# Performance work log

Hardware: AMD Instinct MI355X
Metric: run time of the kernel (lower is better)

The kernel has to match this reference:

```python
import jax, jax.numpy as jnp
import numpy as np

M, N = 63, 127            # parity checks x code length (BCH(127,64))
B = 256                   # base batch of codewords
NUM_SHIFTS = 4            # GL 'num_shifts'
NUM_ITERS = 3             # GL 'num_iterations'
PENALTY = 2.0             # GL 'penalty_weight'
BIG = 1e30

_POS = (2 * np.arange(N)) % N          # Frobenius automorphism i -> 2i mod n
_INV = np.zeros(N, np.int32); _INV[_POS] = np.arange(N)
_STEP = N // NUM_SHIFTS
_SHIFTS = [i * _STEP for i in range(NUM_SHIFTS)]  # deterministic (offset=0)


def setup_inputs() -> dict:
    key = jax.random.key(0)
    k1, k2 = jax.random.split(key)
    soft_input = jax.random.normal(k1, (B, N), dtype=jnp.float32)
    labels = jax.random.randint(k2, (B, N), 0, 2).astype(jnp.int32)
    rng = np.random.default_rng(0)
    Hnp = (rng.random((M, N)) < 0.25).astype(np.float32)
    rows = np.arange(M)
    Hnp[rows, rows % N] = 1.0              # guarantee >=2 ones per check row
    Hnp[rows, (rows + 1) % N] = 1.0
    H = jnp.asarray(Hnp, jnp.float32)
    check_weight = jnp.array([0.421], jnp.float32)
    return {"soft_input": soft_input, "labels": labels, "H": H,
            "check_weight": check_weight}


def _interleave(a, b):
    m, n1 = a.shape
    n2 = b.shape[1]
    if n1 == n2:
        return jnp.stack([a, b], axis=2).reshape(m, n1 + n2)
    inter = jnp.stack([a[:, :n2], b], axis=2).reshape(m, 2 * n2)
    return jnp.concatenate([inter, a[:, n2:]], axis=1)


def _compute_cv(vc, H, check_weight):
    # vc: [Bs, M, N] masked variable->check messages
    sign = jnp.sign((1.0 - H)[None] + vc)
    row_sign = jnp.prod(sign, axis=2, keepdims=True)      # product over row
    result_sign = row_sign * H * sign                     # extrinsic sign
    back = jnp.where(H == 0, -BIG - 1.0, 0.0)[None]
    vabs = jnp.clip(jnp.abs(vc), 0.0, BIG)
    top2 = jax.lax.top_k(-vabs + back, 2)[0]              # [Bs, M, 2]
    min1 = -top2[..., 0:1] * H                            # per-check min
    min2 = -top2[..., 1:2] * H                            # per-check 2nd min
    result = jnp.where(vabs > min1, min1, min2)           # extrinsic min
    return jax.nn.softplus(check_weight) * result * jax.lax.stop_gradient(result_sign)


def _iteration(soft, H, check_weight):
    # build super batch: [orig ; even/odd split ; frobenius perm] x rolled copies
    split = jnp.concatenate([soft[:, 0::2], soft[:, 1::2]], axis=1)
    perm = soft[:, _POS]
    base = jnp.concatenate([soft, split, perm], axis=0)   # [3B, N]
    sup = jnp.concatenate([jnp.roll(base, s, axis=1) for s in _SHIFTS], axis=0)
    vc = sup[:, None, :] * H[None]                        # [3B*S, M, N]
    cv = _compute_cv(vc, H, check_weight)
    temp = jnp.sum(cv, axis=1)                            # [3B*S, N]
    bs = 3 * B
    chunks = [jnp.roll(temp[i * bs:(i + 1) * bs], -_SHIFTS[i], axis=1)
              for i in range(NUM_SHIFTS)]
    t1 = sum(c[:B] for c in chunks)
    t2 = sum(c[B:2 * B] for c in chunks)
    width = (N + 1) // 2
    inter = _interleave(t2[:, :width], t2[:, width:])
    t3 = sum(c[2 * B:] for c in chunks)
    p = t3[:, _INV]                                       # inverse Frobenius
    return soft + (t1 + inter + p) / (3.0 * NUM_SHIFTS)


def _loss(soft, labels_f):
    weight = jnp.where(jnp.sign(soft) != 1.0 - 2.0 * labels_f, PENALTY, 1.0)
    z = -soft
    ce = jnp.maximum(z, 0.0) - z * labels_f + jnp.log1p(jnp.exp(-jnp.abs(z)))
    return jnp.sum(weight * ce)


def reference(soft_input, labels, H, check_weight):
    labels_f = labels.astype(jnp.float32)
    soft = soft_input
    outs = [soft]
    loss = jnp.float32(0.0)
    for _ in range(NUM_ITERS):
        soft = _iteration(soft, H, check_weight)
        outs.append(soft)
        loss = _loss(soft, labels_f)
    return jnp.stack(outs, axis=0), loss
```

## Files before the change

### kernel.cpp

```cpp
#include <hip/hip_runtime.h>
#include <math.h>

#define MM 63
#define NN 127
#define BB 256
#define NIT 3
#define CSR_STRIDE 76
#define CSC_STRIDE 44
#define PQ_STRIDE 65

__device__ float g_partial[BB];

__global__ __launch_bounds__(1024)
void decode_kernel(const float* __restrict__ soft_in,
                   const int* __restrict__ labels,
                   const float* __restrict__ Hg,
                   const float* __restrict__ cw,
                   float* __restrict__ out)
{
    const int b    = blockIdx.x;
    const int tid  = threadIdx.x;
    const int lane = tid & 63;
    const int wid  = tid >> 6;

    __shared__ unsigned char csr[MM][CSR_STRIDE];
    __shared__ unsigned char csc[NN][CSC_STRIDE];
    __shared__ int   row_w2[MM];
    __shared__ int   col_w[NN];
    __shared__ float base0[NN + 1];
    __shared__ float2 pq[8 * PQ_STRIDE];
    __shared__ float tarr[2][NN];
    __shared__ float red2[2];

    for (int task = wid; task < MM + NN; task += 16) {
        unsigned long long below = (1ull << lane) - 1ull;
        if (task < MM) {
            const int m = task;
            csr[m][lane] = 127;
            if (lane < CSR_STRIDE - 64) csr[m][64 + lane] = 127;
            float h0 = Hg[m * NN + lane];
            float h1 = (lane < NN - 64) ? Hg[m * NN + 64 + lane] : 0.0f;
            unsigned long long b0 = __ballot(h0 != 0.0f);
            unsigned long long b1 = __ballot(h1 != 0.0f);
            int c0 = __popcll(b0);
            if (h0 != 0.0f) csr[m][__popcll(b0 & below)] = (unsigned char)lane;
            if (h1 != 0.0f) csr[m][c0 + __popcll(b1 & below)] = (unsigned char)(64 + lane);
            if (lane == 0) row_w2[m] = (c0 + __popcll(b1) + 7) >> 3;
        } else {
            const int c = task - MM;
            if (lane < CSC_STRIDE) csc[c][lane] = 63;
            float hv = (lane < MM) ? Hg[lane * NN + c] : 0.0f;
            unsigned long long bm = __ballot(hv != 0.0f);
            if (hv != 0.0f) csc[c][__popcll(bm & below)] = (unsigned char)lane;
            if (lane == 0) col_w[c] = (__popcll(bm) + 3) >> 2;
        }
    }
    if (tid < NN) {
        float v = soft_in[b * NN + tid];
        base0[tid] = v;
        out[b * NN + tid] = v;
    }
    if (tid == NN) base0[NN] = 1e30f;
    if (tid >= 256 && tid < 264)
        pq[(tid - 256) * PQ_STRIDE + 63] = make_float2(0.0f, 0.0f);
    const float spw = log1pf(expf(cw[0]));
    __syncthreads();

    for (int it = 0; it < NIT; ++it) {
        {
            const int vs    = tid >> 7;
            const int mslot = (tid >> 1) & 63;
            const int half  = tid & 1;
            if (mslot < MM) {
                const int v     = vs >> 2;
                const int shift = (vs & 3) * 31;
                const int H2    = row_w2[mslot];
                const unsigned int* wp = (const unsigned int*)&csr[mslot][0];
                float m1 = 1e30f, m2 = 1e30f;
                unsigned int sbits = 0u;
                for (int w = half * H2, e = 0; e < H2; ++e, ++w) {
                    unsigned int pk = wp[w];
                    #pragma unroll
                    for (int j = 0; j < 4; ++j) {
                        int c = (pk >> (8 * j)) & 255;
                        int idx = c - shift; idx += (idx < 0) ? NN : 0;
                        if (v) { idx <<= 1; idx -= (idx >= NN) ? NN : 0; }
                        idx = (c == 127) ? 127 : idx;
                        float x = base0[idx];
                        float a = fminf(fabsf(x), 1e30f);
                        sbits ^= __float_as_uint(x);
                        m2 = fminf(m2, fmaxf(a, m1));
                        m1 = fminf(m1, a);
                    }
                }
                float om1 = __shfl_xor(m1, 1);
                float om2 = __shfl_xor(m2, 1);
                unsigned int osb = (unsigned int)__shfl_xor((int)sbits, 1);
                float mm2 = fminf(fminf(m2, om2), fmaxf(m1, om1));
                float mm1 = fminf(m1, om1);
                sbits ^= osb;
                float rs = (sbits >> 31) ? -1.0f : 1.0f;
                rs = (mm1 == 0.0f) ? 0.0f : rs;
                if (half == 0)
                    pq[vs * PQ_STRIDE + mslot] = make_float2(rs * mm1, rs * mm2);
            }
        }
        __syncthreads();

        {
            const int v = tid >> 9;
            const int n = (tid >> 2) & 127;
            const int s = tid & 3;
            if (n < NN) {
                int gn = n;
                if (v) { gn <<= 1; gn -= (gn >= NN) ? NN : 0; }
                const float x = base0[gn];
                const float a = fminf(fabsf(x), 1e30f);
                int jcol = n + s * 31; jcol -= (jcol >= NN) ? NN : 0;
                const int C2 = col_w[jcol];
                const unsigned int* wp = (const unsigned int*)&csc[jcol][0];
                const float2* pqs = &pq[((v << 2) | s) * PQ_STRIDE];
                float acc = 0.0f;
                for (int w = 0; w < C2; ++w) {
                    unsigned int pk = wp[w];
                    #pragma unroll
                    for (int e = 0; e < 4; ++e) {
                        int m = (pk >> (8 * e)) & 255;
                        float2 pv = pqs[m];
                        acc += (a > fabsf(pv.x)) ? pv.x : pv.y;
                    }
                }
                acc += __shfl_xor(acc, 1);
                acc += __shfl_xor(acc, 2);
                if (s == 0) {
                    float sx = (x > 0.0f) ? 1.0f : ((x < 0.0f) ? -1.0f : 0.0f);
                    tarr[v][n] = spw * sx * acc;
                }
            }
        }
        __syncthreads();

        if (tid < NN) {
            const int n = tid;
            float t2v = tarr[1][(n * 64) % NN];
            float ns = base0[n] + (tarr[0][n] + 2.0f * t2v) * (1.0f / 12.0f);
            base0[n] = ns;
            out[(size_t)(it + 1) * (BB * NN) + b * NN + n] = ns;
        }
        __syncthreads();
    }

    float term = 0.0f;
    if (tid < NN) {
        float sft = base0[tid];
        float lf  = (float)labels[b * NN + tid];
        float sg  = (sft > 0.0f) ? 1.0f : ((sft < 0.0f) ? -1.0f : 0.0f);
        float w   = (sg != (1.0f - 2.0f * lf)) ? 2.0f : 1.0f;
        float z   = -sft;
        term = w * (fmaxf(z, 0.0f) - z * lf + log1pf(expf(-fabsf(z))));
    }
    if (tid < 128) {
        #pragma unroll
        for (int off = 32; off > 0; off >>= 1)
            term += __shfl_down(term, off);
        if (lane == 0) red2[wid] = term;
    }
    __syncthreads();
    if (tid == 0) g_partial[b] = red2[0] + red2[1];
}

__global__ __launch_bounds__(256)
void loss_kernel(float* __restrict__ out)
{
    __shared__ float red[256];
    const int tid = threadIdx.x;
    red[tid] = g_partial[tid];
    __syncthreads();
    for (int off = 128; off > 0; off >>= 1) {
        if (tid < off) red[tid] += red[tid + off];
        __syncthreads();
    }
    if (tid == 0) out[4 * BB * NN] = red[0];
}

extern "C" void kernel_launch(void* const* d_in, const int* in_sizes, int n_in,
                              void* d_out, int out_size, void* d_ws, size_t ws_size,
                              hipStream_t stream) {
    const float* soft   = (const float*)d_in[0];
    const int*   labels = (const int*)  d_in[1];
    const float* H      = (const float*)d_in[2];
    const float* cw     = (const float*)d_in[3];
    float* outp = (float*)d_out;

    decode_kernel<<<BB, 1024, 0, stream>>>(soft, labels, H, cw, outp);
    loss_kernel<<<1, 256, 0, stream>>>(outp);
}
```

Baseline: 86.24 us.

## Fuse variable update into check gather, build sparse tables with atomics, drop loss kernel

The check-to-variable gather now uses eight threads per variable, covering both the plain and the Frobenius views. Those threads reduce with shuffles and write the updated soft value directly. This removes the tarr staging array and one barrier per iteration. The CSR/CSC tables are now built with shared-memory atomic counters over a flat scan of H instead of per-row and per-column ballots. The separate loss reduction kernel is replaced by a per-block atomicAdd after a memset, which trades a launch for a memset and makes the floating-point summation order nondeterministic.

After: 87.08 us. No clear change (+1.0%).

```diff
diff --git a/kernel.cpp b/kernel.cpp
--- a/kernel.cpp
+++ b/kernel.cpp
@@ -5,11 +5,9 @@
 #define NN 127
 #define BB 256
 #define NIT 3
-#define CSR_STRIDE 76
-#define CSC_STRIDE 44
-#define PQ_STRIDE 65
-
-__device__ float g_partial[BB];
+#define CSRB 76
+#define CSCB 44
+#define PQS 65
 
 __global__ __launch_bounds__(1024)
 void decode_kernel(const float* __restrict__ soft_in,
@@ -18,52 +16,45 @@
                    const float* __restrict__ cw,
                    float* __restrict__ out)
 {
-    const int b    = blockIdx.x;
-    const int tid  = threadIdx.x;
-    const int lane = tid & 63;
-    const int wid  = tid >> 6;
+    const int b   = blockIdx.x;
+    const int tid = threadIdx.x;
 
-    __shared__ unsigned char csr[MM][CSR_STRIDE];
-    __shared__ unsigned char csc[NN][CSC_STRIDE];
-    __shared__ int   row_w2[MM];
-    __shared__ int   col_w[NN];
+    __shared__ unsigned char csr[MM][CSRB];
+    __shared__ unsigned char csc[NN][CSCB];
+    __shared__ int   rcnt[MM], ccnt[NN];
     __shared__ float base0[NN + 1];
-    __shared__ float2 pq[8 * PQ_STRIDE];
-    __shared__ float tarr[2][NN];
+    __shared__ float2 pq[8 * PQS];
     __shared__ float red2[2];
 
-    for (int task = wid; task < MM + NN; task += 16) {
-        unsigned long long below = (1ull << lane) - 1ull;
-        if (task < MM) {
-            const int m = task;
-            csr[m][lane] = 127;
-            if (lane < CSR_STRIDE - 64) csr[m][64 + lane] = 127;
-            float h0 = Hg[m * NN + lane];
-            float h1 = (lane < NN - 64) ? Hg[m * NN + 64 + lane] : 0.0f;
-            unsigned long long b0 = __ballot(h0 != 0.0f);
-            unsigned long long b1 = __ballot(h1 != 0.0f);
-            int c0 = __popcll(b0);
-            if (h0 != 0.0f) csr[m][__popcll(b0 & below)] = (unsigned char)lane;
-            if (h1 != 0.0f) csr[m][c0 + __popcll(b1 & below)] = (unsigned char)(64 + lane);
-            if (lane == 0) row_w2[m] = (c0 + __popcll(b1) + 7) >> 3;
-        } else {
-            const int c = task - MM;
-            if (lane < CSC_STRIDE) csc[c][lane] = 63;
-            float hv = (lane < MM) ? Hg[lane * NN + c] : 0.0f;
-            unsigned long long bm = __ballot(hv != 0.0f);
-            if (hv != 0.0f) csc[c][__popcll(bm & below)] = (unsigned char)lane;
-            if (lane == 0) col_w[c] = (__popcll(bm) + 3) >> 2;
-        }
+    {
+        unsigned int* w1 = (unsigned int*)&csr[0][0];
+        for (int i = tid; i < MM * CSRB / 4; i += 1024) w1[i] = 0x7f7f7f7fu;
+        unsigned int* w2 = (unsigned int*)&csc[0][0];
+        for (int i = tid; i < NN * CSCB / 4; i += 1024) w2[i] = 0x3f3f3f3fu;
     }
+    if (tid < MM) rcnt[tid] = 0;
+    if (tid < NN) ccnt[tid] = 0;
     if (tid < NN) {
         float v = soft_in[b * NN + tid];
         base0[tid] = v;
         out[b * NN + tid] = v;
     }
     if (tid == NN) base0[NN] = 1e30f;
-    if (tid >= 256 && tid < 264)
-        pq[(tid - 256) * PQ_STRIDE + 63] = make_float2(0.0f, 0.0f);
+    if (tid >= 512 && tid < 520)
+        pq[(tid - 512) * PQS + 63] = make_float2(0.0f, 0.0f);
     const float spw = log1pf(expf(cw[0]));
+    __syncthreads();
+
+    for (int i = tid; i < MM * NN; i += 1024) {
+        if (Hg[i] != 0.0f) {
+            int m = i / NN;
+            int c = i - m * NN;
+            int pr = atomicAdd(&rcnt[m], 1);
+            csr[m][pr] = (unsigned char)c;
+            int pc = atomicAdd(&ccnt[c], 1);
+            csc[c][pc] = (unsigned char)m;
+        }
+    }
     __syncthreads();
 
     for (int it = 0; it < NIT; ++it) {
@@ -74,11 +65,11 @@
             if (mslot < MM) {
                 const int v     = vs >> 2;
                 const int shift = (vs & 3) * 31;
-                const int H2    = row_w2[mslot];
+                const int H2    = (rcnt[mslot] + 7) >> 3;
                 const unsigned int* wp = (const unsigned int*)&csr[mslot][0];
                 float m1 = 1e30f, m2 = 1e30f;
                 unsigned int sbits = 0u;
-                for (int w = half * H2, e = 0; e < H2; ++e, ++w) {
+                for (int e = 0, w = half * H2; e < H2; ++e, ++w) {
                     unsigned int pk = wp[w];
                     #pragma unroll
                     for (int j = 0; j < 4; ++j) {
@@ -87,7 +78,7 @@
                         if (v) { idx <<= 1; idx -= (idx >= NN) ? NN : 0; }
                         idx = (c == 127) ? 127 : idx;
                         float x = base0[idx];
-                        float a = fminf(fabsf(x), 1e30f);
+                        float a = fabsf(x);
                         sbits ^= __float_as_uint(x);
                         m2 = fminf(m2, fmaxf(a, m1));
                         m1 = fminf(m1, a);
@@ -99,27 +90,27 @@
                 float mm2 = fminf(fminf(m2, om2), fmaxf(m1, om1));
                 float mm1 = fminf(m1, om1);
                 sbits ^= osb;
-                float rs = (sbits >> 31) ? -1.0f : 1.0f;
+                float rs = (sbits & 0x80000000u) ? -1.0f : 1.0f;
                 rs = (mm1 == 0.0f) ? 0.0f : rs;
                 if (half == 0)
-                    pq[vs * PQ_STRIDE + mslot] = make_float2(rs * mm1, rs * mm2);
+                    pq[vs * PQS + mslot] = make_float2(rs * mm1, rs * mm2);
             }
         }
         __syncthreads();
 
         {
-            const int v = tid >> 9;
-            const int n = (tid >> 2) & 127;
-            const int s = tid & 3;
+            const int n = tid >> 3;
+            const int k = tid & 7;
             if (n < NN) {
-                int gn = n;
-                if (v) { gn <<= 1; gn -= (gn >= NN) ? NN : 0; }
-                const float x = base0[gn];
-                const float a = fminf(fabsf(x), 1e30f);
-                int jcol = n + s * 31; jcol -= (jcol >= NN) ? NN : 0;
-                const int C2 = col_w[jcol];
-                const unsigned int* wp = (const unsigned int*)&csc[jcol][0];
-                const float2* pqs = &pq[((v << 2) | s) * PQ_STRIDE];
+                const int v = k >> 2;
+                const int s = k & 3;
+                const float x = base0[n];
+                const float a = fabsf(x);
+                int p0 = v ? ((n << 6) % NN) : n;
+                int j = p0 + s * 31; j -= (j >= NN) ? NN : 0;
+                const int C2 = (ccnt[j] + 3) >> 2;
+                const unsigned int* wp = (const unsigned int*)&csc[j][0];
+                const float2* pqs = &pq[((v << 2) | s) * PQS];
                 float acc = 0.0f;
                 for (int w = 0; w < C2; ++w) {
                     unsigned int pk = wp[w];
@@ -130,22 +121,17 @@
                         acc += (a > fabsf(pv.x)) ? pv.x : pv.y;
                     }
                 }
+                if (v) acc += acc;
                 acc += __shfl_xor(acc, 1);
                 acc += __shfl_xor(acc, 2);
-                if (s == 0) {
+                acc += __shfl_xor(acc, 4);
+                if (k == 0) {
                     float sx = (x > 0.0f) ? 1.0f : ((x < 0.0f) ? -1.0f : 0.0f);
-                    tarr[v][n] = spw * sx * acc;
+                    float ns = x + spw * sx * acc * (1.0f / 12.0f);
+                    base0[n] = ns;
+                    out[(size_t)(it + 1) * (BB * NN) + b * NN + n] = ns;
                 }
             }
-        }
-        __syncthreads();
-
-        if (tid < NN) {
-            const int n = tid;
-            float t2v = tarr[1][(n * 64) % NN];
-            float ns = base0[n] + (tarr[0][n] + 2.0f * t2v) * (1.0f / 12.0f);
-            base0[n] = ns;
-            out[(size_t)(it + 1) * (BB * NN) + b * NN + n] = ns;
         }
         __syncthreads();
     }
@@ -163,24 +149,10 @@
         #pragma unroll
         for (int off = 32; off > 0; off >>= 1)
             term += __shfl_down(term, off);
-        if (lane == 0) red2[wid] = term;
+        if ((tid & 63) == 0) red2[tid >> 6] = term;
     }
     __syncthreads();
-    if (tid == 0) g_partial[b] = red2[0] + red2[1];
-}
-
-__global__ __launch_bounds__(256)
-void loss_kernel(float* __restrict__ out)
-{
-    __shared__ float red[256];
-    const int tid = threadIdx.x;
-    red[tid] = g_partial[tid];
-    __syncthreads();
-    for (int off = 128; off > 0; off >>= 1) {
-        if (tid < off) red[tid] += red[tid + off];
-        __syncthreads();
-    }
-    if (tid == 0) out[4 * BB * NN] = red[0];
+    if (tid == 0) atomicAdd(&out[4 * BB * NN], red2[0] + red2[1]);
 }
 
 extern "C" void kernel_launch(void* const* d_in, const int* in_sizes, int n_in,
@@ -192,6 +164,6 @@
     const float* cw     = (const float*)d_in[3];
     float* outp = (float*)d_out;
 
+    hipMemsetAsync(outp + 4 * BB * NN, 0, sizeof(float), stream);
     decode_kernel<<<BB, 1024, 0, stream>>>(soft, labels, H, cw, outp);
-    loss_kernel<<<1, 256, 0, stream>>>(outp);
 }
```
